# Kernel optimization log

Hardware: AMD Instinct MI355X
Metric: run time of the kernel (lower is better)

Reference implementation:

```python
import jax, jax.numpy as jnp
import numpy as np

BS, L, S, AMB = 64, 64, 63, 32   # batch, sentence len, opseq steps, ambiguities per step
H, E, V, MLP = 128, 300, 50000, 1024
EPS = 1e-8


def setup_inputs() -> dict:
    key = jax.random.key(0)
    ks = jax.random.split(key, 12)
    u = lambda k, shp: jax.random.uniform(k, shp, dtype=jnp.float32) * 0.1
    return {
        "sentences1": jax.random.randint(ks[0], (BS, L), 0, V, dtype=jnp.int32),
        "operations1": jax.random.randint(ks[1], (BS, S, 2 * AMB), 0, L, dtype=jnp.int32),
        "oopl1": jnp.full((BS,), L + S, dtype=jnp.int32),
        "sentences2": jax.random.randint(ks[2], (BS, L), 0, V, dtype=jnp.int32),
        "operations2": jax.random.randint(ks[3], (BS, S, 2 * AMB), 0, L, dtype=jnp.int32),
        "oopl2": jnp.full((BS,), L + S, dtype=jnp.int32),
        "W": u(ks[4], (5 * H, E)),
        "U": u(ks[5], (5 * H, 2 * H)),
        "b": jnp.zeros((5 * H,), dtype=jnp.float32),
        "energy_u": u(ks[6], (H,)),
        "unk_embedding": u(ks[7], (E,)),
        "word_embeddings": jax.random.normal(ks[8], (V, E), dtype=jnp.float32),
        "A": u(ks[9], (MLP, 4 * H)),
        "a": u(ks[10], (MLP,)),
        "inv_temperature": jnp.float32(1.0),
    }


def _gates(preact, ccL, ccR):
    # preact: [..., 5H]; tree-LSTM cell (i, fL, fR, o, u gates)
    i = jax.nn.sigmoid(preact[..., :H])
    fL = jax.nn.sigmoid(preact[..., H:2 * H])
    fR = jax.nn.sigmoid(preact[..., 2 * H:3 * H])
    o = jax.nn.sigmoid(preact[..., 3 * H:4 * H])
    u = jnp.tanh(preact[..., 4 * H:5 * H])
    c = fL * ccL + fR * ccR + i * u
    h = o * jnp.tanh(c)
    return c, h


def _run_chart(sentences, operations, W, U, b, energy_u, unk_embedding,
               word_embeddings, inv_temperature):
    bs = sentences.shape[0]
    # leaf phase: embed each word, preact = W @ emb + b, ccL = ccR = 0
    emb = jnp.where(sentences[..., None] >= 0,
                    word_embeddings[jnp.clip(sentences, 0)], unk_embedding)  # [bs,L,E]
    preact = jnp.einsum('ble,ge->blg', emb, W) + b                            # [bs,L,5H]
    c, h = _gates(preact, 0.0, 0.0)
    chart = jnp.zeros((bs, L + S, 2 * H), dtype=jnp.float32)
    chart = chart.at[:, :L, :].set(jnp.concatenate([c, h], axis=-1))

    def step(chart, inp):
        ops, pos = inp                                   # ops: [bs, 2*AMB], pos: scalar
        entries = jnp.take_along_axis(chart, ops[:, :, None].astype(jnp.int32), axis=1)
        entries = entries.reshape(bs, AMB, 2, 2 * H)     # [bs, amb, (L,R), 2H]
        ccL = entries[:, :, 0, :H]
        ccR = entries[:, :, 1, :H]
        hh = entries[:, :, :, H:].reshape(bs, AMB, 2 * H)  # concat(hL, hR)
        pre = jnp.einsum('bak,gk->bag', hh, U) + b         # [bs, amb, 5H]
        c, h = _gates(pre, ccL, ccR)
        # cosine similarity of h against energy_u
        hn = jnp.maximum(jnp.sqrt(jnp.sum(h * h, axis=-1)), EPS)
        un = jnp.maximum(jnp.sqrt(jnp.sum(energy_u * energy_u)), EPS)
        e = jnp.einsum('bah,h->ba', h, energy_u) / (hn * un)
        s = jax.nn.softmax(e * inv_temperature, axis=1)    # [bs, amb]
        combined = jnp.concatenate([jnp.einsum('ba,bah->bh', s, c),
                                    jnp.einsum('ba,bah->bh', s, h)], axis=-1)
        chart = jax.lax.dynamic_update_slice(chart, combined[:, None, :], (0, pos, 0))
        return chart, None

    ops_seq = jnp.swapaxes(operations, 0, 1)             # [S, bs, 2*AMB]
    positions = L + jnp.arange(S, dtype=jnp.int32)
    chart, _ = jax.lax.scan(step, chart, (ops_seq, positions))
    return chart


def reference(sentences1, operations1, oopl1, sentences2, operations2, oopl2,
              W, U, b, energy_u, unk_embedding, word_embeddings, A, a,
              inv_temperature):
    chart1 = _run_chart(sentences1, operations1, W, U, b, energy_u,
                        unk_embedding, word_embeddings, inv_temperature)
    chart2 = _run_chart(sentences2, operations2, W, U, b, energy_u,
                        unk_embedding, word_embeddings, inv_temperature)
    bs = chart1.shape[0]
    bidx = jnp.arange(bs)
    s1 = chart1[bidx, oopl1 - 1, H:]                     # final composed h, [bs, H]
    s2 = chart2[bidx, oopl2 - 1, H:]
    u = (s1 - s2) ** 2
    v = s1 * s2
    conc = jnp.concatenate([u, v, s1, s2], axis=1)       # [bs, 4H]
    out = jax.nn.relu(jnp.einsum('jk,ik->ij', A, conc) + a)
    return out
```

## Files before the change

### kernel.cpp

```cpp
#include <hip/hip_runtime.h>
#include <hip/hip_bf16.h>

#define BSZ 64
#define LL  64
#define SS  63
#define AMB 32
#define HH  128
#define EE  300
#define MLPN 1024
#define GG  640
#define K2  256
#define PP  127
#define CROW 272

typedef __attribute__((ext_vector_type(8))) short short8;
typedef __attribute__((ext_vector_type(4))) float f32x4;

__device__ __forceinline__ float sigf(float x) { return 1.f / (1.f + __expf(-x)); }

__device__ __forceinline__ unsigned short f2bf(float x) {
    unsigned int u = __float_as_uint(x);
    u += 0x7fffu + ((u >> 16) & 1u);
    return (unsigned short)(u >> 16);
}
__device__ __forceinline__ float bf2f(short x) {
    return __uint_as_float(((unsigned)(unsigned short)x) << 16);
}

__device__ __forceinline__ short8 cvt8(f32x4 x0, f32x4 x1) {
    short8 v;
    v[0]=(short)f2bf(x0[0]); v[1]=(short)f2bf(x0[1]);
    v[2]=(short)f2bf(x0[2]); v[3]=(short)f2bf(x0[3]);
    v[4]=(short)f2bf(x1[0]); v[5]=(short)f2bf(x1[1]);
    v[6]=(short)f2bf(x1[2]); v[7]=(short)f2bf(x1[3]);
    return v;
}

#define PWT 25600
#define PUT 20480
__global__ void __launch_bounds__(256) prep_kernel(
        const float* __restrict__ W, const float* __restrict__ U,
        short* __restrict__ WTB, short* __restrict__ UTB) {
    int idx = blockIdx.x * 256 + threadIdx.x;
    if (idx < PWT) {
        int g = idx / 40, cc = idx - g * 40;
        int k0 = cc * 8;
        float f[8];
#pragma unroll
        for (int j = 0; j < 8; ++j)
            f[j] = (k0 + j < EE) ? W[(size_t)g * EE + k0 + j] : 0.f;
        short8 v;
#pragma unroll
        for (int j = 0; j < 8; ++j) v[j] = (short)f2bf(f[j]);
        int n = g >> 4, l15 = g & 15;
        int kk = k0 >> 5, quad = (k0 >> 3) & 3;
        *(short8*)(WTB + ((size_t)((n * 10 + kk) * 64 + quad * 16 + l15)) * 8) = v;
    } else if (idx < PWT + PUT) {
        int o = idx - PWT;
        int g = o >> 5, cc = o & 31;
        int k0 = cc * 8;
        f32x4 x0 = *(const f32x4*)(U + (size_t)g * K2 + k0);
        f32x4 x1 = *(const f32x4*)(U + (size_t)g * K2 + k0 + 4);
        int n = g >> 4, l15 = g & 15;
        int kk = k0 >> 5, quad = (k0 >> 3) & 3;
        *(short8*)(UTB + ((size_t)((n * 8 + kk) * 64 + quad * 16 + l15)) * 8) = cvt8(x0, x1);
    }
}

__global__ void __launch_bounds__(1024) leaf_kernel(
        const int* __restrict__ sent1, const int* __restrict__ sent2,
        const short* __restrict__ WTB, const float* __restrict__ bias,
        const float* __restrict__ unk, const float* __restrict__ wemb,
        short* __restrict__ chartG) {
    __shared__ __align__(16) short AsL[2 * 10 * 64 * 8];
    const int tid = threadIdx.x;
    const int blk = blockIdx.x, pair = blk >> 1, half = blk & 1;
    const int ch = pair >> 6, b = pair & 63;
    const int* sent = ch ? sent2 : sent1;
    const int w = tid >> 6, lane = tid & 63, quad = lane >> 4, l15 = lane & 15;

    {
        float ef[2][8];
        int est[2], eso[2];
#pragma unroll
        for (int i = 0; i < 2; ++i) {
            int slot = i * 1024 + tid;
            est[i] = -1;
            if (slot < 1280) {
                int tloc = slot / 40, oct = slot - tloc * 40;
                est[i] = tloc; eso[i] = oct;
                int sid = sent[b * LL + half * 32 + tloc];
                const float* src = (sid >= 0) ? (wemb + (size_t)sid * EE) : unk;
                int k0 = oct * 8;
                if (k0 + 8 <= EE) {
                    f32x4 x0 = *(const f32x4*)(src + k0);
                    f32x4 x1 = *(const f32x4*)(src + k0 + 4);
                    ef[i][0]=x0[0]; ef[i][1]=x0[1]; ef[i][2]=x0[2]; ef[i][3]=x0[3];
                    ef[i][4]=x1[0]; ef[i][5]=x1[1]; ef[i][6]=x1[2]; ef[i][7]=x1[3];
                } else {
#pragma unroll
                    for (int j = 0; j < 8; ++j) ef[i][j] = (k0 + j < EE) ? src[k0 + j] : 0.f;
                }
            }
        }
#pragma unroll
        for (int i = 0; i < 2; ++i) {
            if (est[i] >= 0) {
                int tloc = est[i], oct = eso[i];
                short8 v;
#pragma unroll
                for (int j = 0; j < 8; ++j) v[j] = (short)f2bf(ef[i][j]);
                *(short8*)(AsL + (((tloc >> 4) * 10 + (oct >> 2)) * 64
                                  + ((oct & 3) << 4) + (tloc & 15)) * 8) = v;
            }
        }
    }
    __syncthreads();

    const int mt2 = w & 1, nu = w >> 1;
    f32x4 acc[3] = {};
    short8 bb0[3], bb1[3];
#define LDW(dst, kkv) do { \
    dst[0] = *(const short8*)(WTB + ((size_t)((nu +  0) * 10 + (kkv)) * 64 + lane) * 8); \
    dst[1] = *(const short8*)(WTB + ((size_t)((nu + 24) * 10 + (kkv)) * 64 + lane) * 8); \
    dst[2] = *(const short8*)(WTB + ((size_t)((nu + 32) * 10 + (kkv)) * 64 + lane) * 8); \
} while (0)
    LDW(bb0, 0);
#pragma unroll 1
    for (int kk = 0; kk < 10; kk += 2) {
        LDW(bb1, kk + 1);
        short8 a0 = *(const short8*)(AsL + ((mt2 * 10 + kk) * 64 + lane) * 8);
        acc[0] = __builtin_amdgcn_mfma_f32_16x16x32_bf16(a0, bb0[0], acc[0], 0, 0, 0);
        acc[1] = __builtin_amdgcn_mfma_f32_16x16x32_bf16(a0, bb0[1], acc[1], 0, 0, 0);
        acc[2] = __builtin_amdgcn_mfma_f32_16x16x32_bf16(a0, bb0[2], acc[2], 0, 0, 0);
        if (kk + 2 < 10) LDW(bb0, kk + 2);
        short8 a1 = *(const short8*)(AsL + ((mt2 * 10 + kk + 1) * 64 + lane) * 8);
        acc[0] = __builtin_amdgcn_mfma_f32_16x16x32_bf16(a1, bb1[0], acc[0], 0, 0, 0);
        acc[1] = __builtin_amdgcn_mfma_f32_16x16x32_bf16(a1, bb1[1], acc[1], 0, 0, 0);
        acc[2] = __builtin_amdgcn_mfma_f32_16x16x32_bf16(a1, bb1[2], acc[2], 0, 0, 0);
    }
#undef LDW

    {
        int jc = nu * 16 + l15;
        float bi = bias[jc], bo = bias[3 * HH + jc], bu = bias[4 * HH + jc];
        size_t pb = (size_t)pair * 16384;
#pragma unroll
        for (int r = 0; r < 4; ++r) {
            float cv = sigf(acc[0][r] + bi) * tanhf(acc[2][r] + bu);
            float hv = sigf(acc[1][r] + bo) * tanhf(cv);
            int l = half * 32 + mt2 * 16 + quad * 4 + r;
            chartG[pb + (size_t)l * 256 + jc]      = (short)f2bf(cv);
            chartG[pb + (size_t)l * 256 + HH + jc] = (short)f2bf(hv);
        }
    }
}

__global__ void __launch_bounds__(1024, 4) step_kernel(
        const int* __restrict__ ops1, const int* __restrict__ ops2,
        const int* __restrict__ oopl1, const int* __restrict__ oopl2,
        const short* __restrict__ UTB, const float* __restrict__ bias,
        const float* __restrict__ eu, const float* __restrict__ invt,
        const short* __restrict__ chartG, float* __restrict__ fin) {
    __shared__ __align__(16) short chartL[127 * CROW + 16];
    __shared__ __align__(16) short As2[2 * 8 * 64 * 8];
    __shared__ __align__(16) float chh[32 * 132];
    __shared__ __align__(16) int ops_all[SS * 64];
    __shared__ unsigned long long smask[64];
    __shared__ int live_list[SS];
    __shared__ float e_num[AMB], h2s[AMB], s_w[AMB];
    __shared__ float comb[2][2][HH];
    __shared__ int nl_sh;
    __shared__ float un_sh;

    const int tid = threadIdx.x;
    const int pair = blockIdx.x, ch = pair >> 6, b = pair & 63;
    const int* ops  = ch ? ops2 : ops1;
    const int* oopl = ch ? oopl2 : oopl1;
    const float it = invt[0];
    const int w = tid >> 6, lane = tid & 63, quad = lane >> 4, l15 = lane & 15;

    const int4* cg = (const int4*)(chartG + (size_t)pair * 16384);
    int4 c0 = cg[tid];
    int4 c1 = cg[1024 + tid];
    int4 opv = make_int4(0, 0, 0, 0);
    if (tid < 1008) opv = ((const int4*)(ops + (size_t)b * SS * 64))[tid];
    if (tid < 64) {
        float v = eu[tid] * eu[tid] + eu[tid + 64] * eu[tid + 64];
        for (int off = 32; off >= 1; off >>= 1) v += __shfl_xor(v, off);
        if (tid == 0) un_sh = fmaxf(sqrtf(v), 1e-8f);
    }
#pragma unroll
    for (int i = 0; i < 3; ++i) {
        int idx = i * 1024 + tid;
        if (idx < 2142)
            ((int4*)(chartL + 64 * CROW))[idx] = make_int4(0, 0, 0, 0);
    }
    {
        int r0 = tid >> 5, cq0 = tid & 31;
        *(int4*)(chartL + r0 * CROW + (cq0 << 3)) = c0;
        int t2 = 1024 + tid;
        int r1 = t2 >> 5, cq1 = t2 & 31;
        *(int4*)(chartL + r1 * CROW + (cq1 << 3)) = c1;
    }
    {
        opv.x = min(max(opv.x, 0), PP - 1);
        opv.y = min(max(opv.y, 0), PP - 1);
        opv.z = min(max(opv.z, 0), PP - 1);
        opv.w = min(max(opv.w, 0), PP - 1);
        if (tid < 1008) ((int4*)ops_all)[tid] = opv;

        int t = tid >> 4;
        unsigned long long bit = 0ull;
        if (tid < 1008) {
            int q;
            q = opv.x - LL; if (q >= 0 && q < t) bit |= 1ull << q;
            q = opv.y - LL; if (q >= 0 && q < t) bit |= 1ull << q;
            q = opv.z - LL; if (q >= 0 && q < t) bit |= 1ull << q;
            q = opv.w - LL; if (q >= 0 && q < t) bit |= 1ull << q;
        }
        bit |= __shfl_xor(bit, 1);
        bit |= __shfl_xor(bit, 2);
        bit |= __shfl_xor(bit, 4);
        bit |= __shfl_xor(bit, 8);
        if ((lane & 15) == 0 && t < SS) smask[t] = bit;
    }
    __syncthreads();

    if (w == 0) {
        unsigned long long my = (lane < SS) ? smask[lane] : 0ull;
        unsigned long long m = 0ull;
        int q0 = oopl[b] - 1 - LL;
        if (q0 >= 0) { if (q0 > SS - 1) q0 = SS - 1; m = 1ull << q0; }
        while (true) {
            unsigned long long c = ((m >> lane) & 1ull) ? my : 0ull;
            for (int off = 32; off >= 1; off >>= 1) c |= __shfl_xor(c, off);
            unsigned long long nm = m | c;
            if (nm == m) break;
            m = nm;
        }
        if (lane == 0) {
            int n = 0;
            for (int t = 0; t < SS; ++t)
                if ((m >> t) & 1) live_list[n++] = t;
            nl_sh = n;
        }
    }
    __syncthreads();

    const int nl = nl_sh;
    const float eul = eu[lane], euh = eu[64 + lane];
    const int smt = w & 1, snu = w >> 1;
    const int sjc = snu * 16 + l15;
    const float bi  = bias[sjc],          bfl = bias[HH + sjc];
    const float bfr = bias[2 * HH + sjc], bo  = bias[3 * HH + sjc];
    const float bu  = bias[4 * HH + sjc];

    for (int sidx = 0; sidx < nl; ++sidx) {
        const int t = live_list[sidx];
        const int* oprow = ops_all + t * 64;

        {
            int a = tid >> 5, oct = tid & 31, side = oct >> 4, m8 = oct & 15;
            int row = oprow[2 * a + side];
            short8 v = *(const short8*)(chartL + row * CROW + HH + m8 * 8);
            *(short8*)(As2 + (((a >> 4) * 8 + (oct >> 2)) * 64
                              + ((oct & 3) << 4) + (a & 15)) * 8) = v;
        }
        __syncthreads();

        float cvals[4], hvals[4];
        {
            f32x4 acc[5] = {};
            for (int kk = 0; kk < 8; ++kk) {
                short8 a0 = *(const short8*)(As2 + ((smt * 8 + kk) * 64 + lane) * 8);
#pragma unroll
                for (int s5 = 0; s5 < 5; ++s5) {
                    short8 bv = *(const short8*)(UTB + ((size_t)((snu + 8 * s5) * 8 + kk) * 64 + lane) * 8);
                    acc[s5] = __builtin_amdgcn_mfma_f32_16x16x32_bf16(a0, bv, acc[s5], 0, 0, 0);
                }
            }
#pragma unroll
            for (int r = 0; r < 4; ++r) {
                int a = smt * 16 + quad * 4 + r;
                float ccLv = bf2f(chartL[oprow[2 * a] * CROW + sjc]);
                float ccRv = bf2f(chartL[oprow[2 * a + 1] * CROW + sjc]);
                float cv = sigf(acc[1][r] + bfl) * ccLv
                         + sigf(acc[2][r] + bfr) * ccRv
                         + sigf(acc[0][r] + bi) * tanhf(acc[4][r] + bu);
                float hv = sigf(acc[3][r] + bo) * tanhf(cv);
                cvals[r] = cv; hvals[r] = hv;
                chh[a * 132 + sjc] = hv;
            }
        }
        __syncthreads();

#pragma unroll
        for (int i = 0; i < 2; ++i) {
            int a = w * 2 + i;
            float h0 = chh[a * 132 + lane], h1 = chh[a * 132 + 64 + lane];
            float pe = h0 * eul + h1 * euh;
            float pn = h0 * h0 + h1 * h1;
            for (int off = 32; off >= 1; off >>= 1) {
                pe += __shfl_xor(pe, off);
                pn += __shfl_xor(pn, off);
            }
            if (lane == 0) { e_num[a] = pe; h2s[a] = pn; }
        }
        __syncthreads();

        if (tid < 64) {
            float v = (tid < AMB)
                ? (e_num[tid] / (fmaxf(sqrtf(h2s[tid]), 1e-8f) * un_sh)) * it
                : -3.4e38f;
            float m = v;
            for (int off = 32; off >= 1; off >>= 1) m = fmaxf(m, __shfl_xor(m, off));
            float ex = (tid < AMB) ? __expf(v - m) : 0.f;
            float su = ex;
            for (int off = 32; off >= 1; off >>= 1) su += __shfl_xor(su, off);
            if (tid < AMB) s_w[tid] = ex / su;
        }
        __syncthreads();

        {
            float sc = 0.f, sh = 0.f;
#pragma unroll
            for (int r = 0; r < 4; ++r) {
                int a = smt * 16 + quad * 4 + r;
                float sw = s_w[a];
                sc = fmaf(sw, cvals[r], sc);
                sh = fmaf(sw, hvals[r], sh);
            }
            sc += __shfl_xor(sc, 16); sc += __shfl_xor(sc, 32);
            sh += __shfl_xor(sh, 16); sh += __shfl_xor(sh, 32);
            if (lane < 16) {
                comb[smt][0][sjc] = sc;
                comb[smt][1][sjc] = sh;
            }
        }
        __syncthreads();
        if (tid < K2) {
            int part = tid >> 7, col = tid & 127;
            float val = comb[0][part][col] + comb[1][part][col];
            chartL[(LL + t) * CROW + part * HH + col] = (short)f2bf(val);
        }
        __syncthreads();
    }

    int p = min(max(oopl[b] - 1, 0), PP - 1);
    if (tid < K2)
        fin[(size_t)pair * K2 + tid] = bf2f(chartL[p * CROW + tid]);
}

__global__ void __launch_bounds__(256) mlp_kernel(
        const float* __restrict__ fin,
        const float* __restrict__ A, const float* __restrict__ abias,
        float* __restrict__ out) {
    __shared__ __align__(16) float conc[4][512];
    const int tid = threadIdx.x;
    const int jt = blockIdx.x & 15, bt = blockIdx.x >> 4;

#pragma unroll
    for (int i = 0; i < 2; ++i) {
        int s = i * 256 + tid;
        int bl = s >> 7, kv = s & 127;
        int k0 = kv * 4, sel = k0 >> 7, kk0 = k0 & 127;
        int b = bt * 4 + bl;
        f32x4 s1 = *(const f32x4*)(fin + (size_t)b * K2 + HH + kk0);
        f32x4 s2 = *(const f32x4*)(fin + (size_t)(BSZ + b) * K2 + HH + kk0);
        f32x4 v;
        if (sel == 0)      { f32x4 d = s1 - s2; v = d * d; }
        else if (sel == 1) v = s1 * s2;
        else if (sel == 2) v = s1;
        else               v = s2;
        *(f32x4*)&conc[bl][k0] = v;
    }
    __syncthreads();

    const int jj = tid & 63, bg = tid >> 6;
    const int j = jt * 64 + jj, b = bt * 4 + bg;
    const float* Arow = A + (size_t)j * 512;
    float acc0 = abias[j], acc1 = 0.f;
    for (int k = 0; k < 512; k += 8) {
        f32x4 a0 = *(const f32x4*)(Arow + k);
        f32x4 a1 = *(const f32x4*)(Arow + k + 4);
        f32x4 c0 = *(const f32x4*)&conc[bg][k];
        f32x4 c1 = *(const f32x4*)&conc[bg][k + 4];
#pragma unroll
        for (int u = 0; u < 4; ++u) {
            acc0 = fmaf(a0[u], c0[u], acc0);
            acc1 = fmaf(a1[u], c1[u], acc1);
        }
    }
    out[(size_t)b * MLPN + j] = fmaxf(acc0 + acc1, 0.f);
}

extern "C" void kernel_launch(void* const* d_in, const int* in_sizes, int n_in,
                              void* d_out, int out_size, void* d_ws, size_t ws_size,
                              hipStream_t stream) {
    const int*   sent1 = (const int*)d_in[0];
    const int*   ops1  = (const int*)d_in[1];
    const int*   oopl1 = (const int*)d_in[2];
    const int*   sent2 = (const int*)d_in[3];
    const int*   ops2  = (const int*)d_in[4];
    const int*   oopl2 = (const int*)d_in[5];
    const float* W     = (const float*)d_in[6];
    const float* U     = (const float*)d_in[7];
    const float* bias  = (const float*)d_in[8];
    const float* eu    = (const float*)d_in[9];
    const float* unk   = (const float*)d_in[10];
    const float* wemb  = (const float*)d_in[11];
    const float* A     = (const float*)d_in[12];
    const float* ab    = (const float*)d_in[13];
    const float* invt  = (const float*)d_in[14];
    float* out = (float*)d_out;
    (void)in_sizes; (void)n_in; (void)out_size; (void)ws_size;

    char* ws = (char*)d_ws;
    const size_t WTB_OFF = 0;
    const size_t UTB_OFF = 409600;
    const size_t CHG_OFF = 737280;
    const size_t FIN_OFF = 4931584;
    short* WTB    = (short*)(ws + WTB_OFF);
    short* UTB    = (short*)(ws + UTB_OFF);
    short* chartG = (short*)(ws + CHG_OFF);
    float* fin    = (float*)(ws + FIN_OFF);

    prep_kernel<<<180, 256, 0, stream>>>(W, U, WTB, UTB);

    leaf_kernel<<<256, 1024, 0, stream>>>(sent1, sent2, WTB, bias, unk, wemb, chartG);

    step_kernel<<<128, 1024, 0, stream>>>(ops1, ops2, oopl1, oopl2,
                                          UTB, bias, eu, invt, chartG, fin);

    mlp_kernel<<<256, 256, 0, stream>>>(fin, A, ab, out);
}
```

Measured before the change: 183.6 us.

## Fuse leaf and step kernels with last-block-finishes handoff via atomic counter

Merges the leaf embedding/gate kernel and the sequential chart-step kernel into one launch of 256 blocks. Each block computes half the leaves into both global and shared chart, then an atomic counter per pair picks the second-arriving block to pull the other half from global memory and run the step recurrence, while the first block exits. This removes one kernel launch and the full chart reload from global memory. In exchange it adds a threadfence/atomic handshake and shares the LDS buffers between the two phases.

```diff
diff --git a/kernel.cpp b/kernel.cpp
--- a/kernel.cpp
+++ b/kernel.cpp
@@ -40,7 +40,9 @@
 #define PUT 20480
 __global__ void __launch_bounds__(256) prep_kernel(
         const float* __restrict__ W, const float* __restrict__ U,
-        short* __restrict__ WTB, short* __restrict__ UTB) {
+        short* __restrict__ WTB, short* __restrict__ UTB,
+        int* __restrict__ cnt) {
+    if (blockIdx.x == 0 && threadIdx.x < 128) cnt[threadIdx.x] = 0;
     int idx = blockIdx.x * 256 + threadIdx.x;
     if (idx < PWT) {
         int g = idx / 40, cc = idx - g * 40;
@@ -67,18 +69,53 @@
     }
 }
 
-__global__ void __launch_bounds__(1024) leaf_kernel(
+__global__ void __launch_bounds__(1024, 4) leafstep_kernel(
         const int* __restrict__ sent1, const int* __restrict__ sent2,
-        const short* __restrict__ WTB, const float* __restrict__ bias,
+        const int* __restrict__ ops1, const int* __restrict__ ops2,
+        const int* __restrict__ oopl1, const int* __restrict__ oopl2,
+        const short* __restrict__ WTB, const short* __restrict__ UTB,
+        const float* __restrict__ bias, const float* __restrict__ eu,
+        const float* __restrict__ invt,
         const float* __restrict__ unk, const float* __restrict__ wemb,
-        short* __restrict__ chartG) {
-    __shared__ __align__(16) short AsL[2 * 10 * 64 * 8];
+        short* __restrict__ chartG, float* __restrict__ fin,
+        int* __restrict__ cnt) {
+    __shared__ __align__(16) short chartL[127 * CROW + 16];
+    __shared__ __align__(16) char  bufB[33280];
+    __shared__ __align__(16) int ops_all[SS * 64];
+    __shared__ unsigned long long smask[64];
+    __shared__ int live_list[SS];
+    __shared__ float e_num[AMB], h2s[AMB], s_w[AMB];
+    __shared__ float comb[2][2][HH];
+    __shared__ int nl_sh;
+    __shared__ float un_sh;
+    __shared__ int role_sh;
+
+    short* AsL = (short*)bufB;
+    short* As2 = (short*)bufB;
+    float* chh = (float*)(bufB + 16384);
+
     const int tid = threadIdx.x;
     const int blk = blockIdx.x, pair = blk >> 1, half = blk & 1;
     const int ch = pair >> 6, b = pair & 63;
     const int* sent = ch ? sent2 : sent1;
+    const int* ops  = ch ? ops2 : ops1;
+    const int* oopl = ch ? oopl2 : oopl1;
+    const float it = invt[0];
     const int w = tid >> 6, lane = tid & 63, quad = lane >> 4, l15 = lane & 15;
 
+    int4 opv = make_int4(0, 0, 0, 0);
+    if (tid < 1008) opv = ((const int4*)(ops + (size_t)b * SS * 64))[tid];
+    if (tid < 64) {
+        float v = eu[tid] * eu[tid] + eu[tid + 64] * eu[tid + 64];
+        for (int off = 32; off >= 1; off >>= 1) v += __shfl_xor(v, off);
+        if (tid == 0) un_sh = fmaxf(sqrtf(v), 1e-8f);
+    }
+#pragma unroll
+    for (int i = 0; i < 3; ++i) {
+        int idx = i * 1024 + tid;
+        if (idx < 2142)
+            ((int4*)(chartL + 64 * CROW))[idx] = make_int4(0, 0, 0, 0);
+    }
     {
         float ef[2][8];
         int est[2], eso[2];
@@ -115,94 +152,6 @@
             }
         }
     }
-    __syncthreads();
-
-    const int mt2 = w & 1, nu = w >> 1;
-    f32x4 acc[3] = {};
-    short8 bb0[3], bb1[3];
-#define LDW(dst, kkv) do { \
-    dst[0] = *(const short8*)(WTB + ((size_t)((nu +  0) * 10 + (kkv)) * 64 + lane) * 8); \
-    dst[1] = *(const short8*)(WTB + ((size_t)((nu + 24) * 10 + (kkv)) * 64 + lane) * 8); \
-    dst[2] = *(const short8*)(WTB + ((size_t)((nu + 32) * 10 + (kkv)) * 64 + lane) * 8); \
-} while (0)
-    LDW(bb0, 0);
-#pragma unroll 1
-    for (int kk = 0; kk < 10; kk += 2) {
-        LDW(bb1, kk + 1);
-        short8 a0 = *(const short8*)(AsL + ((mt2 * 10 + kk) * 64 + lane) * 8);
-        acc[0] = __builtin_amdgcn_mfma_f32_16x16x32_bf16(a0, bb0[0], acc[0], 0, 0, 0);
-        acc[1] = __builtin_amdgcn_mfma_f32_16x16x32_bf16(a0, bb0[1], acc[1], 0, 0, 0);
-        acc[2] = __builtin_amdgcn_mfma_f32_16x16x32_bf16(a0, bb0[2], acc[2], 0, 0, 0);
-        if (kk + 2 < 10) LDW(bb0, kk + 2);
-        short8 a1 = *(const short8*)(AsL + ((mt2 * 10 + kk + 1) * 64 + lane) * 8);
-        acc[0] = __builtin_amdgcn_mfma_f32_16x16x32_bf16(a1, bb1[0], acc[0], 0, 0, 0);
-        acc[1] = __builtin_amdgcn_mfma_f32_16x16x32_bf16(a1, bb1[1], acc[1], 0, 0, 0);
-        acc[2] = __builtin_amdgcn_mfma_f32_16x16x32_bf16(a1, bb1[2], acc[2], 0, 0, 0);
-    }
-#undef LDW
-
-    {
-        int jc = nu * 16 + l15;
-        float bi = bias[jc], bo = bias[3 * HH + jc], bu = bias[4 * HH + jc];
-        size_t pb = (size_t)pair * 16384;
-#pragma unroll
-        for (int r = 0; r < 4; ++r) {
-            float cv = sigf(acc[0][r] + bi) * tanhf(acc[2][r] + bu);
-            float hv = sigf(acc[1][r] + bo) * tanhf(cv);
-            int l = half * 32 + mt2 * 16 + quad * 4 + r;
-            chartG[pb + (size_t)l * 256 + jc]      = (short)f2bf(cv);
-            chartG[pb + (size_t)l * 256 + HH + jc] = (short)f2bf(hv);
-        }
-    }
-}
-
-__global__ void __launch_bounds__(1024, 4) step_kernel(
-        const int* __restrict__ ops1, const int* __restrict__ ops2,
-        const int* __restrict__ oopl1, const int* __restrict__ oopl2,
-        const short* __restrict__ UTB, const float* __restrict__ bias,
-        const float* __restrict__ eu, const float* __restrict__ invt,
-        const short* __restrict__ chartG, float* __restrict__ fin) {
-    __shared__ __align__(16) short chartL[127 * CROW + 16];
-    __shared__ __align__(16) short As2[2 * 8 * 64 * 8];
-    __shared__ __align__(16) float chh[32 * 132];
-    __shared__ __align__(16) int ops_all[SS * 64];
-    __shared__ unsigned long long smask[64];
-    __shared__ int live_list[SS];
-    __shared__ float e_num[AMB], h2s[AMB], s_w[AMB];
-    __shared__ float comb[2][2][HH];
-    __shared__ int nl_sh;
-    __shared__ float un_sh;
-
-    const int tid = threadIdx.x;
-    const int pair = blockIdx.x, ch = pair >> 6, b = pair & 63;
-    const int* ops  = ch ? ops2 : ops1;
-    const int* oopl = ch ? oopl2 : oopl1;
-    const float it = invt[0];
-    const int w = tid >> 6, lane = tid & 63, quad = lane >> 4, l15 = lane & 15;
-
-    const int4* cg = (const int4*)(chartG + (size_t)pair * 16384);
-    int4 c0 = cg[tid];
-    int4 c1 = cg[1024 + tid];
-    int4 opv = make_int4(0, 0, 0, 0);
-    if (tid < 1008) opv = ((const int4*)(ops + (size_t)b * SS * 64))[tid];
-    if (tid < 64) {
-        float v = eu[tid] * eu[tid] + eu[tid + 64] * eu[tid + 64];
-        for (int off = 32; off >= 1; off >>= 1) v += __shfl_xor(v, off);
-        if (tid == 0) un_sh = fmaxf(sqrtf(v), 1e-8f);
-    }
-#pragma unroll
-    for (int i = 0; i < 3; ++i) {
-        int idx = i * 1024 + tid;
-        if (idx < 2142)
-            ((int4*)(chartL + 64 * CROW))[idx] = make_int4(0, 0, 0, 0);
-    }
-    {
-        int r0 = tid >> 5, cq0 = tid & 31;
-        *(int4*)(chartL + r0 * CROW + (cq0 << 3)) = c0;
-        int t2 = 1024 + tid;
-        int r1 = t2 >> 5, cq1 = t2 & 31;
-        *(int4*)(chartL + r1 * CROW + (cq1 << 3)) = c1;
-    }
     {
         opv.x = min(max(opv.x, 0), PP - 1);
         opv.y = min(max(opv.y, 0), PP - 1);
@@ -245,6 +194,63 @@
                 if ((m >> t) & 1) live_list[n++] = t;
             nl_sh = n;
         }
+    }
+    {
+        const int mt2 = w & 1, nu = w >> 1;
+        f32x4 acc[3] = {};
+        short8 bb0[3], bb1[3];
+#define LDW(dst, kkv) do { \
+    dst[0] = *(const short8*)(WTB + ((size_t)((nu +  0) * 10 + (kkv)) * 64 + lane) * 8); \
+    dst[1] = *(const short8*)(WTB + ((size_t)((nu + 24) * 10 + (kkv)) * 64 + lane) * 8); \
+    dst[2] = *(const short8*)(WTB + ((size_t)((nu + 32) * 10 + (kkv)) * 64 + lane) * 8); \
+} while (0)
+        LDW(bb0, 0);
+#pragma unroll 1
+        for (int kk = 0; kk < 10; kk += 2) {
+            LDW(bb1, kk + 1);
+            short8 a0 = *(const short8*)(AsL + ((mt2 * 10 + kk) * 64 + lane) * 8);
+            acc[0] = __builtin_amdgcn_mfma_f32_16x16x32_bf16(a0, bb0[0], acc[0], 0, 0, 0);
+            acc[1] = __builtin_amdgcn_mfma_f32_16x16x32_bf16(a0, bb0[1], acc[1], 0, 0, 0);
+            acc[2] = __builtin_amdgcn_mfma_f32_16x16x32_bf16(a0, bb0[2], acc[2], 0, 0, 0);
+            if (kk + 2 < 10) LDW(bb0, kk + 2);
+            short8 a1 = *(const short8*)(AsL + ((mt2 * 10 + kk + 1) * 64 + lane) * 8);
+            acc[0] = __builtin_amdgcn_mfma_f32_16x16x32_bf16(a1, bb1[0], acc[0], 0, 0, 0);
+            acc[1] = __builtin_amdgcn_mfma_f32_16x16x32_bf16(a1, bb1[1], acc[1], 0, 0, 0);
+            acc[2] = __builtin_amdgcn_mfma_f32_16x16x32_bf16(a1, bb1[2], acc[2], 0, 0, 0);
+        }
+#undef LDW
+        int jc = nu * 16 + l15;
+        float bi = bias[jc], bo = bias[3 * HH + jc], bu = bias[4 * HH + jc];
+        size_t pb = (size_t)pair * 16384;
+#pragma unroll
+        for (int r = 0; r < 4; ++r) {
+            float cv = sigf(acc[0][r] + bi) * tanhf(acc[2][r] + bu);
+            float hv = sigf(acc[1][r] + bo) * tanhf(cv);
+            int l = half * 32 + mt2 * 16 + quad * 4 + r;
+            short cb = (short)f2bf(cv), hb = (short)f2bf(hv);
+            chartG[pb + (size_t)l * 256 + jc]      = cb;
+            chartG[pb + (size_t)l * 256 + HH + jc] = hb;
+            chartL[l * CROW + jc]      = cb;
+            chartL[l * CROW + HH + jc] = hb;
+        }
+    }
+    __syncthreads();
+
+    if (tid == 0) {
+        __threadfence();
+        role_sh = atomicAdd(&cnt[pair], 1);
+    }
+    __syncthreads();
+    if (role_sh == 0) return;
+    if (tid == 0) __threadfence();
+    __syncthreads();
+
+    {
+        const int4* sg = (const int4*)(chartG + (size_t)pair * 16384
+                                       + (size_t)(1 - half) * 32 * 256);
+        int4 s0 = sg[tid];
+        int row = (1 - half) * 32 + (tid >> 5), cq = tid & 31;
+        *(int4*)(chartL + row * CROW + (cq << 3)) = s0;
     }
     __syncthreads();
 
@@ -421,17 +427,19 @@
     const size_t UTB_OFF = 409600;
     const size_t CHG_OFF = 737280;
     const size_t FIN_OFF = 4931584;
+    const size_t CNT_OFF = 5062656;
     short* WTB    = (short*)(ws + WTB_OFF);
     short* UTB    = (short*)(ws + UTB_OFF);
     short* chartG = (short*)(ws + CHG_OFF);
     float* fin    = (float*)(ws + FIN_OFF);
-
-    prep_kernel<<<180, 256, 0, stream>>>(W, U, WTB, UTB);
-
-    leaf_kernel<<<256, 1024, 0, stream>>>(sent1, sent2, WTB, bias, unk, wemb, chartG);
-
-    step_kernel<<<128, 1024, 0, stream>>>(ops1, ops2, oopl1, oopl2,
-                                          UTB, bias, eu, invt, chartG, fin);
+    int*   cnt    = (int*)(ws + CNT_OFF);
+
+    prep_kernel<<<180, 256, 0, stream>>>(W, U, WTB, UTB, cnt);
+
+    leafstep_kernel<<<256, 1024, 0, stream>>>(sent1, sent2, ops1, ops2,
+                                              oopl1, oopl2, WTB, UTB,
+                                              bias, eu, invt, unk, wemb,
+                                              chartG, fin, cnt);
 
     mlp_kernel<<<256, 256, 0, stream>>>(fin, A, ab, out);
 }
```

New measurement: 200.9 us. 1.09x slower.
